# Performance work log

Measured on AMD Instinct MI355X. Metric: run time of the kernel, lower is better.

The kernel has to match this reference:

```python
import jax, jax.numpy as jnp
import numpy as np

LAMBDAS = (0.5, 1.0, 5.0)
MAX_NEURONS = 64
RECONFIG = 50
NS = 2  # threshold between normal-equations, full QR, and incremental QR update


def _scn_forward(X, Y, key):
    """Stochastic Configuration Network training: greedy neuron search with
    incremental QR least-squares refit each step. Faithful to SCNUTrain.forward
    (run in float32; original's float32/float64 mixing bug is normalized away)."""
    N, d = X.shape
    C = len(LAMBDAS) * RECONFIG  # candidate pool size per step
    # per-candidate scale, equivalent to torch.hstack of per-lambda blocks
    scale = jnp.repeat(jnp.asarray(LAMBDAS, X.dtype), RECONFIG)  # [C]
    e = Y
    H_cols, W_cols, b_vals = [], [], []
    Q = R = QT = beta = None
    for k in range(MAX_NEURONS):
        key, kw, kb = jax.random.split(key, 3)
        W_random = scale * (2.0 * jax.random.uniform(kw, (d, C), X.dtype) - 1.0)  # [d,C]
        b_random = scale * (2.0 * jax.random.uniform(kb, (1, C), X.dtype) - 1.0)  # [1,C]
        h = jax.nn.sigmoid(X @ W_random + b_random)                 # [N,C]
        v = (e.T @ h) ** 2 / jnp.sum(h * h, axis=0)                 # [m,C]
        best = jnp.argmax(jnp.mean(v, axis=0))
        h_c = jnp.take(h, best, axis=1)                              # [N]
        H_cols.append(h_c)
        W_cols.append(jnp.take(W_random, best, axis=1))
        b_vals.append(jnp.take(b_random[0], best))
        Hk = jnp.stack(H_cols, axis=1)                               # [N,k+1]
        if k < NS:
            beta = jnp.linalg.inv(Hk.T @ Hk) @ (Hk.T @ Y)            # normal equations
        elif k == NS:
            Q, R = jnp.linalg.qr(Hk)                                 # reduced QR: [N,k+1],[k+1,k+1]
            QT = Q.T @ Y                                             # [k+1,m]
            beta = jax.scipy.linalg.solve_triangular(R, QT, lower=False)
        else:
            # incremental Gram-Schmidt QR update with the new column h_c
            r1 = Q.T @ h_c                                           # [k]
            t = h_c - Q @ r1                                         # [N]
            r2 = jnp.linalg.norm(t)
            q = t / r2
            Q = jnp.concatenate([Q, q[:, None]], axis=1)             # [N,k+1]
            top = jnp.concatenate([R, r1[:, None]], axis=1)          # [k,k+1]
            bot = jnp.concatenate([jnp.zeros((k,), X.dtype), r2[None]])[None, :]
            R = jnp.concatenate([top, bot], axis=0)                  # [k+1,k+1]
            QT = jnp.concatenate([QT, (q @ Y)[None, :]], axis=0)     # [k+1,m]
            beta = jax.scipy.linalg.solve_triangular(R, QT, lower=False)
        e = Y - Hk @ beta                                            # residual for next step
    W = jnp.stack(W_cols, axis=1)   # [d, MAX_NEURONS]
    b = jnp.stack(b_vals)           # [MAX_NEURONS]
    return W, b, beta               # beta: [MAX_NEURONS, m]


def setup_inputs() -> dict:
    key = jax.random.key(0)
    kx, ky = jax.random.split(key)
    N, d, m = 10000, 784, 10
    X = jax.random.normal(kx, (N, d), dtype=jnp.float32)
    labels = jax.random.randint(ky, (N,), 0, m)
    Y = jax.nn.one_hot(labels, m, dtype=jnp.float32)
    return {"X": X, "Y": Y}


def reference(X, Y):
    return _scn_forward(X, Y, jax.random.key(42))
```

## Files before the change

kernel.cpp:

```cpp
#include <hip/hip_runtime.h>
#include <cstdint>

#define NROWS 10000
#define DIM   784
#define CAND  150
#define MOUT  10
#define KMAX  64
#define TOT_W 117600
#define TOT_B 150
#define BR 64
#define BC 160
#define KT 16
#define NBLK 157
#define NB256 40

#define RND_(r) { x0 += x1; x1 = (x1 << r) | (x1 >> (32 - r)); x1 ^= x0; }

__device__ __host__ inline void threefry2x32(uint32_t k0, uint32_t k1,
                                             uint32_t c0, uint32_t c1,
                                             uint32_t* o0, uint32_t* o1) {
  uint32_t ks2 = 0x1BD11BDAu ^ k0 ^ k1;
  uint32_t x0 = c0 + k0, x1 = c1 + k1;
  RND_(13) RND_(15) RND_(26) RND_(6)
  x0 += k1;  x1 += ks2 + 1u;
  RND_(17) RND_(29) RND_(16) RND_(24)
  x0 += ks2; x1 += k0 + 2u;
  RND_(13) RND_(15) RND_(26) RND_(6)
  x0 += k0;  x1 += k1 + 3u;
  RND_(17) RND_(29) RND_(16) RND_(24)
  x0 += k1;  x1 += ks2 + 4u;
  RND_(13) RND_(15) RND_(26) RND_(6)
  x0 += ks2; x1 += k0 + 5u;
  *o0 = x0; *o1 = x1;
}

__device__ inline float uni01(uint32_t bits) {
  uint32_t fb = (bits >> 9) | 0x3F800000u;
  return __uint_as_float(fb) - 1.0f;
}

__device__ inline float scale_of(int j) {
  return (j < 50) ? 0.5f : ((j < 100) ? 1.0f : 5.0f);
}

__global__ __launch_bounds__(256) void init_kern(const float* __restrict__ Y, float* __restrict__ e,
                                                 unsigned* __restrict__ counter) {
  int i = blockIdx.x * 256 + threadIdx.x;
  if (i < NROWS * MOUT) e[i] = Y[i];
  if (i == 0) *counter = 0u;
}

__global__ __launch_bounds__(256) void gen_rand_kern(float* __restrict__ Wr, float* __restrict__ br,
                                                     uint32_t kw0, uint32_t kw1,
                                                     uint32_t kb0, uint32_t kb1) {
  int f = blockIdx.x * 256 + threadIdx.x;
  if (f < TOT_W) {
    uint32_t o0, o1;
    threefry2x32(kw0, kw1, 0u, (uint32_t)f, &o0, &o1);
    float u = uni01(o0 ^ o1);
    int j = f % CAND;
    Wr[f] = scale_of(j) * (2.0f * u - 1.0f);
  } else if (f < TOT_W + TOT_B) {
    int g = f - TOT_W;
    uint32_t o0, o1;
    threefry2x32(kb0, kb1, 0u, (uint32_t)g, &o0, &o1);
    float u = uni01(o0 ^ o1);
    br[g] = scale_of(g) * (2.0f * u - 1.0f);
  }
}

__global__ __launch_bounds__(256) void gemm_h_kern(const float* __restrict__ X, const float* __restrict__ e,
                                                   const float* __restrict__ Wr, const float* __restrict__ br_,
                                                   float* __restrict__ h_col, float* __restrict__ part1t) {
  __shared__ __align__(16) float smem[7040];
  __shared__ float et[BR][MOUT];
  float* Xt = smem;
  float* Wt = smem + 1024;
  float* red = smem;

  int tid = threadIdx.x;
  int ty = tid >> 5, tx = tid & 31;
  int row0 = blockIdx.x * BR;
  int nr = NROWS - row0; if (nr > BR) nr = BR;
  bool full = (nr == BR);

  for (int idx = tid; idx < BR * MOUT; idx += 256) {
    int r = idx / MOUT, c = idx - r * MOUT;
    et[r][c] = (row0 + r < NROWS) ? e[(size_t)(row0 + r) * MOUT + c] : 0.f;
  }

  float bbv[5];
#pragma unroll
  for (int cl = 0; cl < 5; ++cl) {
    int c = tx + 32 * cl;
    bbv[cl] = (c < CAND) ? br_[c] : 0.f;
  }

  float acc[8][5];
#pragma unroll
  for (int r = 0; r < 8; ++r)
#pragma unroll
    for (int cl = 0; cl < 5; ++cl) acc[r][cl] = 0.f;

  int rstage = tid >> 2;
  int qg = (tid & 3) * 4;
  int rclamp = rstage < nr ? rstage : nr - 1;
  const float* Xrow = X + (size_t)(row0 + rclamp) * DIM;

  for (int kk = 0; kk < DIM; kk += KT) {
    __syncthreads();
    float4 xv4 = *(const float4*)(Xrow + kk + qg);
    Xt[(qg + 0) * BR + rstage] = xv4.x;
    Xt[(qg + 1) * BR + rstage] = xv4.y;
    Xt[(qg + 2) * BR + rstage] = xv4.z;
    Xt[(qg + 3) * BR + rstage] = xv4.w;
    for (int idx = tid; idx < KT * BC; idx += 256) {
      int q = idx / BC, c = idx - q * BC;
      Wt[idx] = (c < CAND) ? Wr[(size_t)(kk + q) * CAND + c] : 0.f;
    }
    __syncthreads();
#pragma unroll
    for (int q = 0; q < KT; ++q) {
      float xv[8];
      *(float4*)&xv[0] = *(const float4*)&Xt[q * BR + ty * 8];
      *(float4*)&xv[4] = *(const float4*)&Xt[q * BR + ty * 8 + 4];
      float wv[5];
#pragma unroll
      for (int cl = 0; cl < 5; ++cl) wv[cl] = Wt[q * BC + tx + 32 * cl];
#pragma unroll
      for (int r = 0; r < 8; ++r)
#pragma unroll
        for (int cl = 0; cl < 5; ++cl)
          acc[r][cl] = fmaf(xv[r], wv[cl], acc[r][cl]);
    }
  }

  __syncthreads();

#pragma unroll
  for (int cl = 0; cl < 5; ++cl) {
    int c = tx + 32 * cl;
    float hv[8];
#pragma unroll
    for (int r = 0; r < 8; ++r)
      hv[r] = 1.0f / (1.0f + expf(-(acc[r][cl] + bbv[cl])));
    if (c < CAND) {
      float* dst = h_col + (size_t)c * NROWS + row0 + ty * 8;
      if (full) {
        float4 a = {hv[0], hv[1], hv[2], hv[3]};
        float4 b4 = {hv[4], hv[5], hv[6], hv[7]};
        *(float4*)dst = a;
        *(float4*)(dst + 4) = b4;
      } else {
#pragma unroll
        for (int r = 0; r < 8; ++r)
          if (ty * 8 + r < nr) dst[r] = hv[r];
      }
    }
    float hh = 0.f, eth[10];
#pragma unroll
    for (int j = 0; j < 10; ++j) eth[j] = 0.f;
#pragma unroll
    for (int r = 0; r < 8; ++r) {
      if (full || ty * 8 + r < nr) {
        hh = fmaf(hv[r], hv[r], hh);
#pragma unroll
        for (int j = 0; j < 10; ++j) eth[j] = fmaf(et[ty * 8 + r][j], hv[r], eth[j]);
      }
    }
    hh += __shfl_xor(hh, 32);
#pragma unroll
    for (int j = 0; j < 10; ++j) eth[j] += __shfl_xor(eth[j], 32);
    if (!(ty & 1) && c < CAND) {
      float* dstr = red + (ty >> 1) * 1760 + c * 11;
      dstr[0] = hh;
#pragma unroll
      for (int j = 0; j < 10; ++j) dstr[1 + j] = eth[j];
    }
  }
  __syncthreads();
  for (int idx = tid; idx < CAND * 11; idx += 256) {
    float s = red[idx] + red[1760 + idx] + red[3520 + idx] + red[5280 + idx];
    part1t[(size_t)idx * NBLK + blockIdx.x] = s;
  }
}

__global__ __launch_bounds__(64) void score_v_kern(const float* __restrict__ part1t,
                                                   float* __restrict__ vglob) {
  int c = blockIdx.x, tid = threadIdx.x;
  float sums[11];
#pragma unroll
  for (int j = 0; j < 11; ++j) {
    const float* p = part1t + (size_t)(c * 11 + j) * NBLK;
    float s = (tid < NBLK) ? p[tid] : 0.f;
    if (tid + 64 < NBLK) s += p[tid + 64];
    if (tid + 128 < NBLK) s += p[tid + 128];
    s += __shfl_xor(s, 32); s += __shfl_xor(s, 16); s += __shfl_xor(s, 8);
    s += __shfl_xor(s, 4);  s += __shfl_xor(s, 2);  s += __shfl_xor(s, 1);
    sums[j] = s;
  }
  if (tid == 0) {
    float hh = sums[0];
    float accv = 0.f;
#pragma unroll
    for (int j = 0; j < 10; ++j) { float d = sums[1 + j]; accv += (d * d) / hh; }
    vglob[c] = accv / 10.0f;
  }
}

__global__ __launch_bounds__(256) void pick_kern(const float* __restrict__ vglob,
                                                 const float* __restrict__ Wr, const float* __restrict__ br,
                                                 float* __restrict__ outW, float* __restrict__ outb,
                                                 int* __restrict__ ibest, int k) {
  __shared__ float sv[256];
  __shared__ int   si[256];
  __shared__ int   sbest;
  int tid = threadIdx.x;
  float v = -INFINITY; int bi = 0x7FFFFFFF;
  if (tid < CAND) { v = vglob[tid]; bi = tid; }
  sv[tid] = v; si[tid] = bi;
  __syncthreads();
  for (int s2 = 128; s2 > 0; s2 >>= 1) {
    if (tid < s2) {
      float v2 = sv[tid + s2]; int i2 = si[tid + s2];
      if (v2 > sv[tid] || (v2 == sv[tid] && i2 < si[tid])) { sv[tid] = v2; si[tid] = i2; }
    }
    __syncthreads();
  }
  if (tid == 0) { sbest = si[0]; *ibest = si[0]; }
  __syncthreads();
  int best = sbest;
  for (int i = tid; i < DIM; i += 256) outW[(size_t)i * KMAX + k] = Wr[(size_t)i * CAND + best];
  if (tid == 0) outb[k] = br[best];
}

__global__ __launch_bounds__(256) void qr_r1_kern(const float* __restrict__ h_col, float* __restrict__ Hm,
                                                  const float* __restrict__ Qm, float* __restrict__ r1g,
                                                  const int* __restrict__ ibest, int k) {
  int j = blockIdx.x, tid = threadIdx.x;
  int best = *ibest;
  const float* hc = h_col + (size_t)best * NROWS;
  if (j == k) {
    for (int i = tid; i < NROWS; i += 256)
      Hm[(size_t)k * NROWS + i] = hc[i];
  } else {
    float local = 0.f;
    for (int i = tid; i < NROWS; i += 256)
      local = fmaf(Qm[(size_t)j * NROWS + i], hc[i], local);
    local += __shfl_xor(local, 32); local += __shfl_xor(local, 16);
    local += __shfl_xor(local, 8);  local += __shfl_xor(local, 4);
    local += __shfl_xor(local, 2);  local += __shfl_xor(local, 1);
    __shared__ float wred[4];
    int wid = tid >> 6, lane = tid & 63;
    if (lane == 0) wred[wid] = local;
    __syncthreads();
    if (tid == 0) r1g[j] = wred[0] + wred[1] + wred[2] + wred[3];
  }
}

__global__ __launch_bounds__(256) void qr_tf_kern(const float* __restrict__ Hm, float* __restrict__ Qm,
                                                  const float* __restrict__ r1g, const float* __restrict__ Y,
                                                  float* __restrict__ part2, float* __restrict__ Rm,
                                                  float* __restrict__ QT, float* __restrict__ scal,
                                                  float* __restrict__ outBeta, unsigned* __restrict__ counter,
                                                  int k) {
  __shared__ float r1s[KMAX];
  int tid = threadIdx.x;
  for (int jj = tid; jj < k; jj += 256) r1s[jj] = r1g[jj];
  __syncthreads();

  int i = blockIdx.x * 256 + tid;
  float tval = 0.f, hc = 0.f, h0 = 0.f;
  float yv[10];
#pragma unroll
  for (int c = 0; c < 10; ++c) yv[c] = 0.f;

  if (i < NROWS) {
    hc = Hm[(size_t)k * NROWS + i];
    float s = 0.f;
    for (int jj = 0; jj < k; ++jj) s = fmaf(Qm[(size_t)jj * NROWS + i], r1s[jj], s);
    tval = hc - s;
    Qm[(size_t)k * NROWS + i] = tval;
#pragma unroll
    for (int c = 0; c < 10; ++c) yv[c] = Y[(size_t)i * 10 + c];
    if (k == 1) h0 = Hm[i];
  }

  float p[23];
  p[0] = tval * tval;
#pragma unroll
  for (int c = 0; c < 10; ++c) p[1 + c] = tval * yv[c];
  p[11] = hc * hc;
  p[12] = h0 * hc;
#pragma unroll
  for (int c = 0; c < 10; ++c) p[13 + c] = hc * yv[c];

  __shared__ float wred[4][23];
  int lane = tid & 63, wid = tid >> 6;
#pragma unroll
  for (int c = 0; c < 23; ++c) {
    float v = p[c];
    v += __shfl_xor(v, 32); v += __shfl_xor(v, 16); v += __shfl_xor(v, 8);
    v += __shfl_xor(v, 4);  v += __shfl_xor(v, 2);  v += __shfl_xor(v, 1);
    if (lane == 0) wred[wid][c] = v;
  }
  __syncthreads();
  if (tid < 23) part2[blockIdx.x * 23 + tid] = wred[0][tid] + wred[1][tid] + wred[2][tid] + wred[3][tid];

  __syncthreads();
  __shared__ int lastFlag;
  if (tid == 0) {
    __threadfence();
    unsigned d = __hip_atomic_fetch_add(counter, 1u, __ATOMIC_ACQ_REL, __HIP_MEMORY_SCOPE_AGENT);
    lastFlag = (d == NB256 - 1) ? 1 : 0;
  }
  __syncthreads();
  if (!lastFlag) return;
  if (tid == 0) { __threadfence(); *counter = 0u; }
  __syncthreads();

  __shared__ float vals[23];
  __shared__ float bsh[KMAX * 10];
  if (tid < 23) {
    float s = 0.f;
    for (int b = 0; b < NB256; ++b) s += part2[b * 23 + tid];
    vals[tid] = s;
  }
  __syncthreads();
  float r2 = sqrtf(vals[0]);
  if (tid < k) Rm[tid * KMAX + k] = r1g[tid];
  if (tid == 0) { Rm[k * KMAX + k] = r2; scal[0] = r2; }
  if (tid < 10) QT[k * 10 + tid] = vals[1 + tid] / r2;
  if (k == 0 && tid < 11) scal[1 + tid] = vals[tid];
  __syncthreads();
  if (k == 0) {
    if (tid < 10) outBeta[tid] = (1.0f / vals[0]) * vals[1 + tid];
  } else if (k == 1) {
    if (tid < 10) {
      float g00 = scal[1], g0y = scal[2 + tid];
      float s11 = vals[11], s01 = vals[12], s1y = vals[13 + tid];
      float det = g00 * s11 - s01 * s01;
      float i00 = s11 / det, i01 = -s01 / det, i11 = g00 / det;
      outBeta[tid]      = i00 * g0y + i01 * s1y;
      outBeta[10 + tid] = i01 * g0y + i11 * s1y;
    }
  } else {
    if (tid < 10) {
      for (int row = k; row >= 0; --row) {
        float s = QT[row * 10 + tid];
        for (int jj = row + 1; jj <= k; ++jj) s = fmaf(-Rm[row * KMAX + jj], bsh[jj * 10 + tid], s);
        float bv = s / Rm[row * KMAX + row];
        bsh[row * 10 + tid] = bv;
        outBeta[row * 10 + tid] = bv;
      }
    }
  }
}

__global__ __launch_bounds__(256) void upd_gen_kern(const float* __restrict__ Hm, float* __restrict__ Qm,
                                                    const float* __restrict__ Y, const float* __restrict__ beta,
                                                    float* __restrict__ e, const float* __restrict__ scal,
                                                    float* __restrict__ Wr, float* __restrict__ br,
                                                    uint32_t kw0, uint32_t kw1, uint32_t kb0, uint32_t kb1,
                                                    int k) {
  int b = blockIdx.x, tid = threadIdx.x;
  if (b < NB256) {
    int i = b * 256 + tid;
    if (i >= NROWS) return;
    float r2 = scal[0];
    Qm[(size_t)k * NROWS + i] = Qm[(size_t)k * NROWS + i] / r2;
    float s[10];
#pragma unroll
    for (int c = 0; c < 10; ++c) s[c] = 0.f;
    for (int j = 0; j <= k; ++j) {
      float hv = Hm[(size_t)j * NROWS + i];
#pragma unroll
      for (int c = 0; c < 10; ++c) s[c] = fmaf(hv, beta[j * 10 + c], s[c]);
    }
#pragma unroll
    for (int c = 0; c < 10; ++c) e[(size_t)i * 10 + c] = Y[(size_t)i * 10 + c] - s[c];
  } else {
    int f = (b - NB256) * 256 + tid;
    if (f < TOT_W) {
      uint32_t o0, o1;
      threefry2x32(kw0, kw1, 0u, (uint32_t)f, &o0, &o1);
      float u = uni01(o0 ^ o1);
      int j = f % CAND;
      Wr[f] = scale_of(j) * (2.0f * u - 1.0f);
    } else if (f < TOT_W + TOT_B) {
      int g = f - TOT_W;
      uint32_t o0, o1;
      threefry2x32(kb0, kb1, 0u, (uint32_t)g, &o0, &o1);
      float u = uni01(o0 ^ o1);
      br[g] = scale_of(g) * (2.0f * u - 1.0f);
    }
  }
}

extern "C" void kernel_launch(void* const* d_in, const int* in_sizes, int n_in,
                              void* d_out, int out_size, void* d_ws, size_t ws_size,
                              hipStream_t stream) {
  const float* X = (const float*)d_in[0];
  const float* Y = (const float*)d_in[1];
  float* out = (float*)d_out;
  float* outW    = out;
  float* outb    = out + (size_t)DIM * KMAX;
  float* outBeta = outb + KMAX;

  float* ws = (float*)d_ws;
  size_t off = 0;
  float* h_col = ws + off; off += (size_t)NROWS * CAND;
  float* Wr    = ws + off; off += TOT_W;
  float* br    = ws + off; off += 256;
  float* e     = ws + off; off += (size_t)NROWS * MOUT;
  float* Hm    = ws + off; off += (size_t)KMAX * NROWS;
  float* Qm    = ws + off; off += (size_t)KMAX * NROWS;
  float* Rm    = ws + off; off += (size_t)KMAX * KMAX;
  float* QT    = ws + off; off += (size_t)KMAX * MOUT;
  float* r1g   = ws + off; off += KMAX;
  float* part1t = ws + off; off += (size_t)CAND * 11 * NBLK;
  float* part2  = ws + off; off += (size_t)NB256 * 23;
  float* vglob  = ws + off; off += 256;
  float* scal   = ws + off; off += 16;
  int*   ibest  = (int*)(ws + off); off += 4;
  unsigned* counter = (unsigned*)(ws + off); off += 4;

  uint32_t kws0[KMAX], kws1[KMAX], kbs0[KMAX], kbs1[KMAX];
  uint32_t key0 = 0u, key1 = 42u;
  for (int k = 0; k < KMAX; ++k) {
    uint32_t o0[3], o1[3];
    for (int t = 0; t < 3; ++t)
      threefry2x32(key0, key1, 0u, (uint32_t)t, &o0[t], &o1[t]);
    kws0[k] = o0[1]; kws1[k] = o1[1]; kbs0[k] = o0[2]; kbs1[k] = o1[2];
    key0 = o0[0]; key1 = o1[0];
  }

  init_kern<<<(NROWS * MOUT + 255) / 256, 256, 0, stream>>>(Y, e, counter);
  gen_rand_kern<<<(TOT_W + TOT_B + 255) / 256, 256, 0, stream>>>(Wr, br, kws0[0], kws1[0], kbs0[0], kbs1[0]);

  for (int k = 0; k < KMAX; ++k) {
    gemm_h_kern<<<NBLK, 256, 0, stream>>>(X, e, Wr, br, h_col, part1t);
    score_v_kern<<<CAND, 64, 0, stream>>>(part1t, vglob);
    pick_kern<<<1, 256, 0, stream>>>(vglob, Wr, br, outW, outb, ibest, k);
    qr_r1_kern<<<k + 1, 256, 0, stream>>>(h_col, Hm, Qm, r1g, ibest, k);
    qr_tf_kern<<<NB256, 256, 0, stream>>>(Hm, Qm, r1g, Y, part2, Rm, QT, scal, outBeta, counter, k);
    bool genNext = (k + 1 < KMAX);
    int nblocks = genNext ? (NB256 + (TOT_W + TOT_B + 255) / 256) : NB256;
    int kn = genNext ? (k + 1) : 0;
    upd_gen_kern<<<nblocks, 256, 0, stream>>>(Hm, Qm, Y, outBeta, e, scal, Wr, br,
                                              kws0[kn], kws1[kn], kbs0[kn], kbs1[kn], k);
  }
}
```

Measured before the change: 19.55 ms.

## Fuse per-step pipeline into two kernels with last-block reductions and lazy Q normalization

Collapses the six per-neuron launches into two kernels. Scoring, argmax and weight selection move into the GEMM kernel through a last-block-done atomic counter. The residual e is recomputed inside the GEMM blocks from H and beta instead of being stored. The Q column is left unnormalized, with scaling folded into coefficients via a stored r2. The QR projection runs in a single kernel alongside generation of the next step's random weights. This cuts launch overhead and global round trips, at the cost of a serial tail in the last block and redundant residual computation per GEMM block.

```diff
diff --git a/kernel.cpp b/kernel.cpp
--- a/kernel.cpp
+++ b/kernel.cpp
@@ -12,7 +12,8 @@
 #define BC 160
 #define KT 16
 #define NBLK 157
-#define NB256 40
+#define NTB 40
+#define GENB 460
 
 #define RND_(r) { x0 += x1; x1 = (x1 << r) | (x1 >> (32 - r)); x1 ^= x0; }
 
@@ -43,17 +44,8 @@
   return (j < 50) ? 0.5f : ((j < 100) ? 1.0f : 5.0f);
 }
 
-__global__ __launch_bounds__(256) void init_kern(const float* __restrict__ Y, float* __restrict__ e,
-                                                 unsigned* __restrict__ counter) {
-  int i = blockIdx.x * 256 + threadIdx.x;
-  if (i < NROWS * MOUT) e[i] = Y[i];
-  if (i == 0) *counter = 0u;
-}
-
-__global__ __launch_bounds__(256) void gen_rand_kern(float* __restrict__ Wr, float* __restrict__ br,
-                                                     uint32_t kw0, uint32_t kw1,
-                                                     uint32_t kb0, uint32_t kb1) {
-  int f = blockIdx.x * 256 + threadIdx.x;
+__device__ inline void gen_one(int f, uint32_t kw0, uint32_t kw1, uint32_t kb0, uint32_t kb1,
+                               float* __restrict__ Wr, float* __restrict__ br) {
   if (f < TOT_W) {
     uint32_t o0, o1;
     threefry2x32(kw0, kw1, 0u, (uint32_t)f, &o0, &o1);
@@ -69,11 +61,27 @@
   }
 }
 
-__global__ __launch_bounds__(256) void gemm_h_kern(const float* __restrict__ X, const float* __restrict__ e,
-                                                   const float* __restrict__ Wr, const float* __restrict__ br_,
-                                                   float* __restrict__ h_col, float* __restrict__ part1t) {
+__global__ __launch_bounds__(64) void init_kern(unsigned* __restrict__ counters) {
+  if (threadIdx.x < 2) counters[threadIdx.x] = 0u;
+}
+
+__global__ __launch_bounds__(256) void gen_rand_kern(float* __restrict__ Wr, float* __restrict__ br,
+                                                     uint32_t kw0, uint32_t kw1,
+                                                     uint32_t kb0, uint32_t kb1) {
+  int f = blockIdx.x * 256 + threadIdx.x;
+  gen_one(f, kw0, kw1, kb0, kb1, Wr, br);
+}
+
+__global__ __launch_bounds__(256) void gemm_score_kern(
+    const float* __restrict__ X, const float* __restrict__ Y,
+    const float* __restrict__ Hm, const float* __restrict__ beta,
+    const float* __restrict__ Wr, const float* __restrict__ br_,
+    float* __restrict__ h_col, float* __restrict__ part1t,
+    float* __restrict__ outW, float* __restrict__ outb, int* __restrict__ ibest,
+    unsigned* __restrict__ counter, int kprev, int k) {
   __shared__ __align__(16) float smem[7040];
   __shared__ float et[BR][MOUT];
+  __shared__ int lastFlag;
   float* Xt = smem;
   float* Wt = smem + 1024;
   float* red = smem;
@@ -84,9 +92,23 @@
   int nr = NROWS - row0; if (nr > BR) nr = BR;
   bool full = (nr == BR);
 
-  for (int idx = tid; idx < BR * MOUT; idx += 256) {
-    int r = idx / MOUT, c = idx - r * MOUT;
-    et[r][c] = (row0 + r < NROWS) ? e[(size_t)(row0 + r) * MOUT + c] : 0.f;
+  if (tid < BR) {
+    int row = row0 + tid;
+    if (row < NROWS) {
+      float s[10];
+#pragma unroll
+      for (int c = 0; c < 10; ++c) s[c] = 0.f;
+      for (int j = 0; j <= kprev; ++j) {
+        float hv = Hm[(size_t)j * NROWS + row];
+#pragma unroll
+        for (int c = 0; c < 10; ++c) s[c] = fmaf(hv, beta[j * 10 + c], s[c]);
+      }
+#pragma unroll
+      for (int c = 0; c < 10; ++c) et[tid][c] = Y[(size_t)row * MOUT + c] - s[c];
+    } else {
+#pragma unroll
+      for (int c = 0; c < 10; ++c) et[tid][c] = 0.f;
+    }
   }
 
   float bbv[5];
@@ -183,153 +205,146 @@
     float s = red[idx] + red[1760 + idx] + red[3520 + idx] + red[5280 + idx];
     part1t[(size_t)idx * NBLK + blockIdx.x] = s;
   }
-}
-
-__global__ __launch_bounds__(64) void score_v_kern(const float* __restrict__ part1t,
-                                                   float* __restrict__ vglob) {
-  int c = blockIdx.x, tid = threadIdx.x;
-  float sums[11];
-#pragma unroll
-  for (int j = 0; j < 11; ++j) {
-    const float* p = part1t + (size_t)(c * 11 + j) * NBLK;
-    float s = (tid < NBLK) ? p[tid] : 0.f;
-    if (tid + 64 < NBLK) s += p[tid + 64];
-    if (tid + 128 < NBLK) s += p[tid + 128];
+
+  __syncthreads();
+  if (tid == 0) {
+    __threadfence();
+    unsigned d = __hip_atomic_fetch_add(counter, 1u, __ATOMIC_ACQ_REL, __HIP_MEMORY_SCOPE_AGENT);
+    lastFlag = (d == NBLK - 1) ? 1 : 0;
+  }
+  __syncthreads();
+  if (!lastFlag) return;
+  if (tid == 0) { __threadfence(); *counter = 0u; }
+
+  float* sums = smem;
+  float* vbuf = smem + 1664;
+  __shared__ int sbest;
+  for (int idx = tid; idx < CAND * 11; idx += 256) {
+    const float* p = part1t + (size_t)idx * NBLK;
+    float s = 0.f;
+    for (int b2 = 0; b2 < NBLK; ++b2) s += p[b2];
+    sums[idx] = s;
+  }
+  __syncthreads();
+  if (tid < CAND) {
+    float hh = sums[tid * 11];
+    float accv = 0.f;
+#pragma unroll
+    for (int c = 0; c < 10; ++c) { float d = sums[tid * 11 + 1 + c]; accv += (d * d) / hh; }
+    vbuf[tid] = accv / 10.0f;
+  }
+  __syncthreads();
+  if (tid == 0) {
+    float bv = vbuf[0]; int bi = 0;
+    for (int c = 1; c < CAND; ++c) {
+      float v = vbuf[c];
+      if (v > bv) { bv = v; bi = c; }
+    }
+    sbest = bi; *ibest = bi; outb[k] = br_[bi];
+  }
+  __syncthreads();
+  int best = sbest;
+  for (int i = tid; i < DIM; i += 256) outW[(size_t)i * KMAX + k] = Wr[(size_t)i * CAND + best];
+}
+
+__global__ __launch_bounds__(256) void qrall_kern(
+    const float* __restrict__ h_col, const float* __restrict__ Y,
+    float* __restrict__ Hm, float* __restrict__ Qm, float* __restrict__ r2g,
+    float* __restrict__ Rm, float* __restrict__ QT, float* __restrict__ scal,
+    float* __restrict__ outBeta, float* __restrict__ part2,
+    const int* __restrict__ ibest, unsigned* __restrict__ counter,
+    float* __restrict__ Wr, float* __restrict__ br,
+    uint32_t kw0, uint32_t kw1, uint32_t kb0, uint32_t kb1, int k) {
+  int b = blockIdx.x, tid = threadIdx.x;
+  if (b >= NTB) {
+    int f = (b - NTB) * 256 + tid;
+    gen_one(f, kw0, kw1, kb0, kb1, Wr, br);
+    return;
+  }
+
+  __shared__ float r1s[KMAX];
+  __shared__ float coef[KMAX];
+  __shared__ float wred[4][23];
+  __shared__ int lastFlag;
+  int best = *ibest;
+  const float* hc_g = h_col + (size_t)best * NROWS;
+
+  int i = b * 256 + tid;
+  if (i < NROWS) Hm[(size_t)k * NROWS + i] = hc_g[i];
+
+  int wid = tid >> 6, lane = tid & 63;
+  for (int j = wid; j < k; j += 4) {
+    const float* tj = Qm + (size_t)j * NROWS;
+    float s = 0.f;
+    for (int ii = lane; ii < NROWS; ii += 64)
+      s = fmaf(tj[ii], hc_g[ii], s);
     s += __shfl_xor(s, 32); s += __shfl_xor(s, 16); s += __shfl_xor(s, 8);
     s += __shfl_xor(s, 4);  s += __shfl_xor(s, 2);  s += __shfl_xor(s, 1);
-    sums[j] = s;
-  }
-  if (tid == 0) {
-    float hh = sums[0];
-    float accv = 0.f;
-#pragma unroll
-    for (int j = 0; j < 10; ++j) { float d = sums[1 + j]; accv += (d * d) / hh; }
-    vglob[c] = accv / 10.0f;
-  }
-}
-
-__global__ __launch_bounds__(256) void pick_kern(const float* __restrict__ vglob,
-                                                 const float* __restrict__ Wr, const float* __restrict__ br,
-                                                 float* __restrict__ outW, float* __restrict__ outb,
-                                                 int* __restrict__ ibest, int k) {
-  __shared__ float sv[256];
-  __shared__ int   si[256];
-  __shared__ int   sbest;
-  int tid = threadIdx.x;
-  float v = -INFINITY; int bi = 0x7FFFFFFF;
-  if (tid < CAND) { v = vglob[tid]; bi = tid; }
-  sv[tid] = v; si[tid] = bi;
-  __syncthreads();
-  for (int s2 = 128; s2 > 0; s2 >>= 1) {
-    if (tid < s2) {
-      float v2 = sv[tid + s2]; int i2 = si[tid + s2];
-      if (v2 > sv[tid] || (v2 == sv[tid] && i2 < si[tid])) { sv[tid] = v2; si[tid] = i2; }
-    }
-    __syncthreads();
-  }
-  if (tid == 0) { sbest = si[0]; *ibest = si[0]; }
-  __syncthreads();
-  int best = sbest;
-  for (int i = tid; i < DIM; i += 256) outW[(size_t)i * KMAX + k] = Wr[(size_t)i * CAND + best];
-  if (tid == 0) outb[k] = br[best];
-}
-
-__global__ __launch_bounds__(256) void qr_r1_kern(const float* __restrict__ h_col, float* __restrict__ Hm,
-                                                  const float* __restrict__ Qm, float* __restrict__ r1g,
-                                                  const int* __restrict__ ibest, int k) {
-  int j = blockIdx.x, tid = threadIdx.x;
-  int best = *ibest;
-  const float* hc = h_col + (size_t)best * NROWS;
-  if (j == k) {
-    for (int i = tid; i < NROWS; i += 256)
-      Hm[(size_t)k * NROWS + i] = hc[i];
-  } else {
-    float local = 0.f;
-    for (int i = tid; i < NROWS; i += 256)
-      local = fmaf(Qm[(size_t)j * NROWS + i], hc[i], local);
-    local += __shfl_xor(local, 32); local += __shfl_xor(local, 16);
-    local += __shfl_xor(local, 8);  local += __shfl_xor(local, 4);
-    local += __shfl_xor(local, 2);  local += __shfl_xor(local, 1);
-    __shared__ float wred[4];
-    int wid = tid >> 6, lane = tid & 63;
-    if (lane == 0) wred[wid] = local;
-    __syncthreads();
-    if (tid == 0) r1g[j] = wred[0] + wred[1] + wred[2] + wred[3];
-  }
-}
-
-__global__ __launch_bounds__(256) void qr_tf_kern(const float* __restrict__ Hm, float* __restrict__ Qm,
-                                                  const float* __restrict__ r1g, const float* __restrict__ Y,
-                                                  float* __restrict__ part2, float* __restrict__ Rm,
-                                                  float* __restrict__ QT, float* __restrict__ scal,
-                                                  float* __restrict__ outBeta, unsigned* __restrict__ counter,
-                                                  int k) {
-  __shared__ float r1s[KMAX];
-  int tid = threadIdx.x;
-  for (int jj = tid; jj < k; jj += 256) r1s[jj] = r1g[jj];
-  __syncthreads();
-
-  int i = blockIdx.x * 256 + tid;
+    if (lane == 0) {
+      float r2j = r2g[j];
+      float r1j = s / r2j;
+      r1s[j] = r1j;
+      coef[j] = r1j / r2j;
+    }
+  }
+  __syncthreads();
+
   float tval = 0.f, hc = 0.f, h0 = 0.f;
   float yv[10];
 #pragma unroll
   for (int c = 0; c < 10; ++c) yv[c] = 0.f;
-
   if (i < NROWS) {
-    hc = Hm[(size_t)k * NROWS + i];
+    hc = hc_g[i];
     float s = 0.f;
-    for (int jj = 0; jj < k; ++jj) s = fmaf(Qm[(size_t)jj * NROWS + i], r1s[jj], s);
+    for (int jj = 0; jj < k; ++jj) s = fmaf(Qm[(size_t)jj * NROWS + i], coef[jj], s);
     tval = hc - s;
     Qm[(size_t)k * NROWS + i] = tval;
 #pragma unroll
-    for (int c = 0; c < 10; ++c) yv[c] = Y[(size_t)i * 10 + c];
+    for (int c = 0; c < 10; ++c) yv[c] = Y[(size_t)i * MOUT + c];
     if (k == 1) h0 = Hm[i];
   }
 
+  int np = (k == 1) ? 23 : 11;
   float p[23];
   p[0] = tval * tval;
 #pragma unroll
   for (int c = 0; c < 10; ++c) p[1 + c] = tval * yv[c];
-  p[11] = hc * hc;
-  p[12] = h0 * hc;
-#pragma unroll
-  for (int c = 0; c < 10; ++c) p[13 + c] = hc * yv[c];
-
-  __shared__ float wred[4][23];
-  int lane = tid & 63, wid = tid >> 6;
-#pragma unroll
-  for (int c = 0; c < 23; ++c) {
+  if (k == 1) {
+    p[11] = hc * hc;
+    p[12] = h0 * hc;
+#pragma unroll
+    for (int c = 0; c < 10; ++c) p[13 + c] = hc * yv[c];
+  }
+  for (int c = 0; c < np; ++c) {
     float v = p[c];
     v += __shfl_xor(v, 32); v += __shfl_xor(v, 16); v += __shfl_xor(v, 8);
     v += __shfl_xor(v, 4);  v += __shfl_xor(v, 2);  v += __shfl_xor(v, 1);
     if (lane == 0) wred[wid][c] = v;
   }
   __syncthreads();
-  if (tid < 23) part2[blockIdx.x * 23 + tid] = wred[0][tid] + wred[1][tid] + wred[2][tid] + wred[3][tid];
-
-  __syncthreads();
-  __shared__ int lastFlag;
+  if (tid < np) part2[b * 23 + tid] = wred[0][tid] + wred[1][tid] + wred[2][tid] + wred[3][tid];
+
+  __syncthreads();
   if (tid == 0) {
     __threadfence();
     unsigned d = __hip_atomic_fetch_add(counter, 1u, __ATOMIC_ACQ_REL, __HIP_MEMORY_SCOPE_AGENT);
-    lastFlag = (d == NB256 - 1) ? 1 : 0;
+    lastFlag = (d == NTB - 1) ? 1 : 0;
   }
   __syncthreads();
   if (!lastFlag) return;
   if (tid == 0) { __threadfence(); *counter = 0u; }
-  __syncthreads();
 
   __shared__ float vals[23];
   __shared__ float bsh[KMAX * 10];
-  if (tid < 23) {
+  if (tid < np) {
     float s = 0.f;
-    for (int b = 0; b < NB256; ++b) s += part2[b * 23 + tid];
+    for (int b2 = 0; b2 < NTB; ++b2) s += part2[b2 * 23 + tid];
     vals[tid] = s;
   }
   __syncthreads();
   float r2 = sqrtf(vals[0]);
-  if (tid < k) Rm[tid * KMAX + k] = r1g[tid];
-  if (tid == 0) { Rm[k * KMAX + k] = r2; scal[0] = r2; }
+  if (tid < k) Rm[tid * KMAX + k] = r1s[tid];
+  if (tid == 0) { Rm[k * KMAX + k] = r2; r2g[k] = r2; }
   if (tid < 10) QT[k * 10 + tid] = vals[1 + tid] / r2;
   if (k == 0 && tid < 11) scal[1 + tid] = vals[tid];
   __syncthreads();
@@ -357,46 +372,6 @@
   }
 }
 
-__global__ __launch_bounds__(256) void upd_gen_kern(const float* __restrict__ Hm, float* __restrict__ Qm,
-                                                    const float* __restrict__ Y, const float* __restrict__ beta,
-                                                    float* __restrict__ e, const float* __restrict__ scal,
-                                                    float* __restrict__ Wr, float* __restrict__ br,
-                                                    uint32_t kw0, uint32_t kw1, uint32_t kb0, uint32_t kb1,
-                                                    int k) {
-  int b = blockIdx.x, tid = threadIdx.x;
-  if (b < NB256) {
-    int i = b * 256 + tid;
-    if (i >= NROWS) return;
-    float r2 = scal[0];
-    Qm[(size_t)k * NROWS + i] = Qm[(size_t)k * NROWS + i] / r2;
-    float s[10];
-#pragma unroll
-    for (int c = 0; c < 10; ++c) s[c] = 0.f;
-    for (int j = 0; j <= k; ++j) {
-      float hv = Hm[(size_t)j * NROWS + i];
-#pragma unroll
-      for (int c = 0; c < 10; ++c) s[c] = fmaf(hv, beta[j * 10 + c], s[c]);
-    }
-#pragma unroll
-    for (int c = 0; c < 10; ++c) e[(size_t)i * 10 + c] = Y[(size_t)i * 10 + c] - s[c];
-  } else {
-    int f = (b - NB256) * 256 + tid;
-    if (f < TOT_W) {
-      uint32_t o0, o1;
-      threefry2x32(kw0, kw1, 0u, (uint32_t)f, &o0, &o1);
-      float u = uni01(o0 ^ o1);
-      int j = f % CAND;
-      Wr[f] = scale_of(j) * (2.0f * u - 1.0f);
-    } else if (f < TOT_W + TOT_B) {
-      int g = f - TOT_W;
-      uint32_t o0, o1;
-      threefry2x32(kb0, kb1, 0u, (uint32_t)g, &o0, &o1);
-      float u = uni01(o0 ^ o1);
-      br[g] = scale_of(g) * (2.0f * u - 1.0f);
-    }
-  }
-}
-
 extern "C" void kernel_launch(void* const* d_in, const int* in_sizes, int n_in,
                               void* d_out, int out_size, void* d_ws, size_t ws_size,
                               hipStream_t stream) {
@@ -412,18 +387,16 @@
   float* h_col = ws + off; off += (size_t)NROWS * CAND;
   float* Wr    = ws + off; off += TOT_W;
   float* br    = ws + off; off += 256;
-  float* e     = ws + off; off += (size_t)NROWS * MOUT;
   float* Hm    = ws + off; off += (size_t)KMAX * NROWS;
   float* Qm    = ws + off; off += (size_t)KMAX * NROWS;
   float* Rm    = ws + off; off += (size_t)KMAX * KMAX;
   float* QT    = ws + off; off += (size_t)KMAX * MOUT;
-  float* r1g   = ws + off; off += KMAX;
+  float* r2g   = ws + off; off += KMAX;
   float* part1t = ws + off; off += (size_t)CAND * 11 * NBLK;
-  float* part2  = ws + off; off += (size_t)NB256 * 23;
-  float* vglob  = ws + off; off += 256;
+  float* part2  = ws + off; off += (size_t)NTB * 23;
   float* scal   = ws + off; off += 16;
   int*   ibest  = (int*)(ws + off); off += 4;
-  unsigned* counter = (unsigned*)(ws + off); off += 4;
+  unsigned* counters = (unsigned*)(ws + off); off += 4;
 
   uint32_t kws0[KMAX], kws1[KMAX], kbs0[KMAX], kbs1[KMAX];
   uint32_t key0 = 0u, key1 = 42u;
@@ -435,19 +408,18 @@
     key0 = o0[0]; key1 = o1[0];
   }
 
-  init_kern<<<(NROWS * MOUT + 255) / 256, 256, 0, stream>>>(Y, e, counter);
+  init_kern<<<1, 64, 0, stream>>>(counters);
   gen_rand_kern<<<(TOT_W + TOT_B + 255) / 256, 256, 0, stream>>>(Wr, br, kws0[0], kws1[0], kbs0[0], kbs1[0]);
 
   for (int k = 0; k < KMAX; ++k) {
-    gemm_h_kern<<<NBLK, 256, 0, stream>>>(X, e, Wr, br, h_col, part1t);
-    score_v_kern<<<CAND, 64, 0, stream>>>(part1t, vglob);
-    pick_kern<<<1, 256, 0, stream>>>(vglob, Wr, br, outW, outb, ibest, k);
-    qr_r1_kern<<<k + 1, 256, 0, stream>>>(h_col, Hm, Qm, r1g, ibest, k);
-    qr_tf_kern<<<NB256, 256, 0, stream>>>(Hm, Qm, r1g, Y, part2, Rm, QT, scal, outBeta, counter, k);
+    gemm_score_kern<<<NBLK, 256, 0, stream>>>(X, Y, Hm, outBeta, Wr, br,
+                                              h_col, part1t, outW, outb, ibest,
+                                              &counters[0], k - 1, k);
     bool genNext = (k + 1 < KMAX);
-    int nblocks = genNext ? (NB256 + (TOT_W + TOT_B + 255) / 256) : NB256;
+    int nb = genNext ? (NTB + GENB) : NTB;
     int kn = genNext ? (k + 1) : 0;
-    upd_gen_kern<<<nblocks, 256, 0, stream>>>(Hm, Qm, Y, outBeta, e, scal, Wr, br,
-                                              kws0[kn], kws1[kn], kbs0[kn], kbs1[kn], k);
-  }
-}
+    qrall_kern<<<nb, 256, 0, stream>>>(h_col, Y, Hm, Qm, r2g, Rm, QT, scal,
+                                       outBeta, part2, ibest, &counters[1],
+                                       Wr, br, kws0[kn], kws1[kn], kbs0[kn], kbs1[kn], k);
+  }
+}
```

Result: slower. 49.81 ms (+154.8%).
